# Kernel optimization log

Measured on AMD Instinct MI355X. Metric: run time of the kernel, lower is better.

## Reference

```python
import jax, jax.numpy as jnp
from jax import lax
import numpy as np

FEAT = 256
B = 16
T = 4096
BETA = 1.0


def setup_inputs() -> dict:
    key = jax.random.key(0)
    k0, k1, k2 = jax.random.split(key, 3)
    encoder_outputs = jax.random.normal(k0, (B, T, FEAT), dtype=jnp.float32)
    # Conv1d weight: (out_ch, in_ch, kernel)
    conv_w = jax.random.normal(k1, (FEAT, FEAT, 5), dtype=jnp.float32) * 0.02
    conv_b = jnp.zeros((FEAT,), dtype=jnp.float32)
    lin_w = jax.random.normal(k2, (FEAT, 1), dtype=jnp.float32) * 0.05
    lin_b = jnp.zeros((1,), dtype=jnp.float32)
    return {"encoder_outputs": encoder_outputs, "conv_w": conv_w,
            "conv_b": conv_b, "lin_w": lin_w, "lin_b": lin_b}


def _alphas(x, conv_w, conv_b, lin_w, lin_b):
    # x: [B, T, D] -> alphas [B, T]
    xc = jnp.transpose(x, (0, 2, 1))  # NCH
    y = lax.conv_general_dilated(xc, conv_w, window_strides=(1,),
                                 padding='SAME',
                                 dimension_numbers=('NCH', 'OIH', 'NCH'))
    y = y + conv_b[None, :, None]
    y = jnp.transpose(y, (0, 2, 1))  # [B, T, D]
    return jax.nn.sigmoid(y @ lin_w + lin_b)[..., 0]  # [B, T]


def _cif_single(alpha, h, beta):
    # alpha: [T], h: [T, D]  integrate-and-fire scan
    D = h.shape[-1]
    Tlen = alpha.shape[0]

    def step(carry, inp):
        acc, hacc = carry
        a, hu = inp
        acc_new = acc + a
        fire = acc_new >= beta
        a1 = 1.0 - acc          # mass to complete current segment
        c = hacc + a1 * hu      # emitted segment vector (if fired)
        a2 = a - a1             # leftover mass starting next segment
        acc_out = jnp.where(fire, a2, acc_new)
        hacc_out = jnp.where(fire, a2 * hu, hacc + a * hu)
        return (acc_out, hacc_out), (fire, jnp.where(fire, c, jnp.zeros_like(c)))

    init = (jnp.zeros((), h.dtype), jnp.zeros((D,), h.dtype))
    (acc_f, hacc_f), (fires, cs) = lax.scan(step, init, (alpha, h))

    # pack fired emissions densely; non-fired steps scatter into dump slot Tlen
    idx = jnp.cumsum(fires.astype(jnp.int32)) - 1
    idx = jnp.where(fires, idx, Tlen)
    out = jnp.zeros((Tlen + 1, D), h.dtype).at[idx].add(cs)[:Tlen]
    n = fires.sum().astype(jnp.int32)
    # if no segment fired, emit the final accumulator (torch: c=[h_accum[-1]])
    out = out.at[0].set(jnp.where(n == 0, hacc_f, out[0]))
    n = jnp.maximum(n, 1)
    return out, n


def reference(encoder_outputs, conv_w, conv_b, lin_w, lin_b):
    alphas = _alphas(encoder_outputs, conv_w, conv_b, lin_w, lin_b)  # [B, T]
    out_c, len_tensor = jax.vmap(lambda a, h: _cif_single(a, h, BETA))(
        alphas, encoder_outputs)
    return out_c, len_tensor
```

## Files before the change

kernel.cpp:

```cpp
#include <hip/hip_runtime.h>
#include <math.h>

#define FEAT 256
#define NB   16
#define TLEN 4096
#define NROWS (NB * TLEN)

#define OFF_WEFF 0
#define OFF_BEFF 1280
#define OFF_P    2048
#define OFF_W1   (OFF_P + 5 * NROWS)
#define OFF_W2   (OFF_W1 + NROWS)
#define OFF_FPOS (OFF_W2 + NROWS)
#define OFF_NF   (OFF_FPOS + NROWS)
#define OFF_PART (OFF_NF + 16)
#define OFF_ALPHA (OFF_PART + 8 * 1280)
#define OFF_CSUM (OFF_ALPHA + NROWS)

__global__ __launch_bounds__(256) void weff1_kernel(
    const float* __restrict__ conv_w, const float* __restrict__ lin_w,
    float* __restrict__ ws) {
  int ob = blockIdx.x % 5, oc = blockIdx.x / 5;
  int idx = ob * 256 + threadIdx.x;
  float acc = 0.f;
  int o0 = oc * 32;
#pragma unroll 8
  for (int o = o0; o < o0 + 32; ++o)
    acc = fmaf(conv_w[o * (FEAT * 5) + idx], lin_w[o], acc);
  ws[OFF_PART + oc * 1280 + idx] = acc;
}

__global__ __launch_bounds__(256) void weff2_kernel(
    const float* __restrict__ conv_b, const float* __restrict__ lin_w,
    const float* __restrict__ lin_b, float* __restrict__ ws) {
  if (blockIdx.x < 5) {
    int idx = blockIdx.x * 256 + threadIdx.x;
    float acc = 0.f;
#pragma unroll
    for (int c = 0; c < 8; ++c) acc += ws[OFF_PART + c * 1280 + idx];
    int i = idx / 5, k = idx - i * 5;
    ws[OFF_WEFF + k * FEAT + i] = acc;
  } else {
    __shared__ float red[256];
    red[threadIdx.x] = conv_b[threadIdx.x] * lin_w[threadIdx.x];
    __syncthreads();
    for (int s = 128; s > 0; s >>= 1) {
      if (threadIdx.x < s) red[threadIdx.x] += red[threadIdx.x + s];
      __syncthreads();
    }
    if (threadIdx.x == 0) ws[OFF_BEFF] = red[0] + lin_b[0];
  }
}

__global__ __launch_bounds__(256) void pdot_kernel(
    const float* __restrict__ x, float* __restrict__ ws) {
  int tid  = threadIdx.x;
  int wave = tid >> 6, l = tid & 63;
  int row  = blockIdx.x * 32 + wave * 8 + (l >> 3);
  int l8   = l & 7;
  const float* xr = x + (size_t)row * FEAT + l8 * 4;
  float p[5] = {0.f, 0.f, 0.f, 0.f, 0.f};
#pragma unroll
  for (int pass = 0; pass < 8; ++pass) {
    float4 xv = *(const float4*)(xr + pass * 32);
#pragma unroll
    for (int k = 0; k < 5; ++k) {
      float4 w4 = *(const float4*)(ws + OFF_WEFF + k * FEAT + pass * 32 + l8 * 4);
      p[k] = fmaf(xv.x, w4.x, fmaf(xv.y, w4.y,
              fmaf(xv.z, w4.z, fmaf(xv.w, w4.w, p[k]))));
    }
  }
#pragma unroll
  for (int k = 0; k < 5; ++k) {
    p[k] += __shfl_xor(p[k], 1);
    p[k] += __shfl_xor(p[k], 2);
    p[k] += __shfl_xor(p[k], 4);
  }
  if (l8 == 0) {
#pragma unroll
    for (int k = 0; k < 5; ++k) ws[OFF_P + (size_t)k * NROWS + row] = p[k];
  }
}

__global__ __launch_bounds__(256) void scanA_kernel(float* __restrict__ ws) {
  const int b = blockIdx.x >> 4, chunk = blockIdx.x & 15;
  const int tid = threadIdx.x;
  const int t = chunk * 256 + tid;
  float z = ws[OFF_BEFF];
#pragma unroll
  for (int k = 0; k < 5; ++k) {
    int tt = t + k - 2;
    if (tt >= 0 && tt < TLEN) z += ws[OFF_P + (size_t)k * NROWS + b * TLEN + tt];
  }
  float a = 1.f / (1.f + expf(-z));
  ws[OFF_ALPHA + b * TLEN + t] = a;

  __shared__ double sS[256];
  sS[tid] = (double)a;
  __syncthreads();
  for (int s = 1; s < 256; s <<= 1) {
    double add = (tid >= s) ? sS[tid - s] : 0.0;
    __syncthreads();
    sS[tid] += add;
    __syncthreads();
  }
  if (tid == 255)
    ((double*)ws)[OFF_CSUM / 2 + b * 16 + chunk] = sS[255];
}

__global__ __launch_bounds__(256) void scanB_kernel(
    float* __restrict__ ws, float* __restrict__ out) {
  const int b = blockIdx.x >> 4, chunk = blockIdx.x & 15;
  const int tid = threadIdx.x;
  const int t = chunk * 256 + tid;
  const double* csum = (const double*)ws + OFF_CSUM / 2 + b * 16;
  double offset = 0.0;
  for (int c = 0; c < chunk; ++c) offset += csum[c];

  double a = (double)ws[OFF_ALPHA + b * TLEN + t];
  __shared__ double sS[256];
  sS[tid] = a;
  __syncthreads();
  for (int s = 1; s < 256; s <<= 1) {
    double add = (tid >= s) ? sS[tid - s] : 0.0;
    __syncthreads();
    sS[tid] += add;
    __syncthreads();
  }
  double St = offset + sS[tid];
  double Sp = tid ? offset + sS[tid - 1] : offset;
  double Ft = floor(St), Fp = floor(Sp);

  ws[OFF_W1 + b * TLEN + t] = (float)(fmin(St, Fp + 1.0) - Sp);
  if (Ft > Fp) {
    ws[OFF_W2 + b * TLEN + t] = (float)(St - Ft);
    ((int*)ws)[OFF_FPOS + b * TLEN + (int)Ft - 1] = t;
  }
  if (chunk == 15 && tid == 255) {
    int n = (int)Ft;
    ((int*)ws)[OFF_NF + b] = n;
    out[(size_t)NROWS * FEAT + b] = (float)(n > 0 ? n : 1);
  }
}

__global__ __launch_bounds__(256) void emit_kernel(
    const float* __restrict__ x, const float* __restrict__ ws,
    float* __restrict__ out) {
  int gtid = blockIdx.x * 256 + threadIdx.x;
  int row  = gtid >> 6;
  int lane = gtid & 63;
  int b = row >> 12;
  int j = row & (TLEN - 1);
  int n = ((const int*)ws)[OFF_NF + b];
  int keep = n > 0 ? n : 1;
  float4 acc = make_float4(0.f, 0.f, 0.f, 0.f);
  if (j < keep) {
    const int* fpos = (const int*)ws + OFF_FPOS + b * TLEN;
    int t_lo = j ? fpos[j - 1] : 0;
    int t_hi = (j < n) ? fpos[j] : TLEN - 1;
    const float* w1 = ws + OFF_W1 + b * TLEN;
    const float* w2 = ws + OFF_W2 + b * TLEN;
    for (int t = t_lo; t <= t_hi; ++t) {
      float w = (j && t == t_lo) ? w2[t] : w1[t];
      float4 xv = *(const float4*)(x + ((size_t)b * TLEN + t) * FEAT + lane * 4);
      acc.x = fmaf(w, xv.x, acc.x);
      acc.y = fmaf(w, xv.y, acc.y);
      acc.z = fmaf(w, xv.z, acc.z);
      acc.w = fmaf(w, xv.w, acc.w);
    }
  }
  *(float4*)(out + (size_t)row * FEAT + lane * 4) = acc;
}

extern "C" void kernel_launch(void* const* d_in, const int* in_sizes, int n_in,
                              void* d_out, int out_size, void* d_ws, size_t ws_size,
                              hipStream_t stream) {
  const float* x      = (const float*)d_in[0];
  const float* conv_w = (const float*)d_in[1];
  const float* conv_b = (const float*)d_in[2];
  const float* lin_w  = (const float*)d_in[3];
  const float* lin_b  = (const float*)d_in[4];
  float* out = (float*)d_out;
  float* ws  = (float*)d_ws;

  hipLaunchKernelGGL(weff1_kernel, dim3(40), dim3(256), 0, stream,
                     conv_w, lin_w, ws);
  hipLaunchKernelGGL(weff2_kernel, dim3(6), dim3(256), 0, stream,
                     conv_b, lin_w, lin_b, ws);
  hipLaunchKernelGGL(pdot_kernel, dim3(NROWS / 32), dim3(256), 0, stream, x, ws);
  hipLaunchKernelGGL(scanA_kernel, dim3(NB * 16), dim3(256), 0, stream, ws);
  hipLaunchKernelGGL(scanB_kernel, dim3(NB * 16), dim3(256), 0, stream, ws, out);
  hipLaunchKernelGGL(emit_kernel, dim3(NROWS / 4), dim3(256), 0, stream, x, ws, out);
}
```

Before: 154.8 us.

## Fuse weight reduction, conv-dot and sigmoid; single-block per-batch scan

Merges the bias reduction into the first weight kernel. The partial-sum reduction moves into a new kernel that computes the 5-tap dot products for a 128-row tile with halo, applies the conv window and sigmoid in shared memory, and writes alpha directly, removing the P buffer round trip. The two-pass chunked scan is replaced by one 1024-thread block per batch scanning all 4096 elements in shared memory in double precision. This cuts the launch count from 6 to 4 and removes intermediate global traffic. In exchange, halo rows are reread, each block redundantly re-reduces the weights, and the scan runs on only 16 blocks with 12 log-steps of block-wide barriers.

```diff
diff --git a/kernel.cpp b/kernel.cpp
--- a/kernel.cpp
+++ b/kernel.cpp
@@ -6,40 +6,27 @@
 #define TLEN 4096
 #define NROWS (NB * TLEN)
 
-#define OFF_WEFF 0
-#define OFF_BEFF 1280
-#define OFF_P    2048
-#define OFF_W1   (OFF_P + 5 * NROWS)
-#define OFF_W2   (OFF_W1 + NROWS)
-#define OFF_FPOS (OFF_W2 + NROWS)
-#define OFF_NF   (OFF_FPOS + NROWS)
-#define OFF_PART (OFF_NF + 16)
+#define OFF_BEFF  0
+#define OFF_PART  2
 #define OFF_ALPHA (OFF_PART + 8 * 1280)
-#define OFF_CSUM (OFF_ALPHA + NROWS)
+#define OFF_W1    (OFF_ALPHA + NROWS)
+#define OFF_W2    (OFF_W1 + NROWS)
+#define OFF_FPOS  (OFF_W2 + NROWS)
+#define OFF_NF    (OFF_FPOS + NROWS)
 
 __global__ __launch_bounds__(256) void weff1_kernel(
-    const float* __restrict__ conv_w, const float* __restrict__ lin_w,
+    const float* __restrict__ conv_w, const float* __restrict__ conv_b,
+    const float* __restrict__ lin_w, const float* __restrict__ lin_b,
     float* __restrict__ ws) {
-  int ob = blockIdx.x % 5, oc = blockIdx.x / 5;
-  int idx = ob * 256 + threadIdx.x;
-  float acc = 0.f;
-  int o0 = oc * 32;
+  if (blockIdx.x < 40) {
+    int ob = blockIdx.x % 5, oc = blockIdx.x / 5;
+    int idx = ob * 256 + threadIdx.x;
+    float acc = 0.f;
+    int o0 = oc * 32;
 #pragma unroll 8
-  for (int o = o0; o < o0 + 32; ++o)
-    acc = fmaf(conv_w[o * (FEAT * 5) + idx], lin_w[o], acc);
-  ws[OFF_PART + oc * 1280 + idx] = acc;
-}
-
-__global__ __launch_bounds__(256) void weff2_kernel(
-    const float* __restrict__ conv_b, const float* __restrict__ lin_w,
-    const float* __restrict__ lin_b, float* __restrict__ ws) {
-  if (blockIdx.x < 5) {
-    int idx = blockIdx.x * 256 + threadIdx.x;
-    float acc = 0.f;
-#pragma unroll
-    for (int c = 0; c < 8; ++c) acc += ws[OFF_PART + c * 1280 + idx];
-    int i = idx / 5, k = idx - i * 5;
-    ws[OFF_WEFF + k * FEAT + i] = acc;
+    for (int o = o0; o < o0 + 32; ++o)
+      acc = fmaf(conv_w[o * (FEAT * 5) + idx], lin_w[o], acc);
+    ws[OFF_PART + oc * 1280 + idx] = acc;
   } else {
     __shared__ float red[256];
     red[threadIdx.x] = conv_b[threadIdx.x] * lin_w[threadIdx.x];
@@ -52,94 +39,127 @@
   }
 }
 
-__global__ __launch_bounds__(256) void pdot_kernel(
+__global__ __launch_bounds__(256) void pdalpha_kernel(
     const float* __restrict__ x, float* __restrict__ ws) {
-  int tid  = threadIdx.x;
-  int wave = tid >> 6, l = tid & 63;
-  int row  = blockIdx.x * 32 + wave * 8 + (l >> 3);
-  int l8   = l & 7;
-  const float* xr = x + (size_t)row * FEAT + l8 * 4;
-  float p[5] = {0.f, 0.f, 0.f, 0.f, 0.f};
-#pragma unroll
-  for (int pass = 0; pass < 8; ++pass) {
-    float4 xv = *(const float4*)(xr + pass * 32);
+  __shared__ float sW[5 * 256];
+  __shared__ float sP[5 * 132];
+  const int tid = threadIdx.x;
+
+#pragma unroll
+  for (int j = 0; j < 5; ++j) {
+    int idx = j * 256 + tid;
+    float acc = 0.f;
+#pragma unroll
+    for (int c = 0; c < 8; ++c) acc += ws[OFF_PART + c * 1280 + idx];
+    int i = idx / 5, k = idx - i * 5;
+    sW[k * 256 + i] = acc;
+  }
+  const float b_eff = ws[OFF_BEFF];
+  __syncthreads();
+
+  const int t0 = blockIdx.x * 128;
+  const int bs = (t0 >> 12) << 12;
+  const int be = bs + TLEN;
+  const int lo = t0 - 2;
+  const int start = lo < bs ? bs : lo;
+  const int end0  = t0 + 130;
+  const int end   = end0 > be ? be : end0;
+  const int cnt   = end - start;
+
+  const int wave = tid >> 6, l = tid & 63, l8 = l & 7, g8 = l >> 3;
+  float p[5][5];
+#pragma unroll
+  for (int rp = 0; rp < 5; ++rp)
+#pragma unroll
+    for (int k = 0; k < 5; ++k) p[rp][k] = 0.f;
+
+  int j0 = wave * 8 + g8;
+#pragma unroll
+  for (int fp = 0; fp < 8; ++fp) {
+    float4 w4[5];
+#pragma unroll
+    for (int k = 0; k < 5; ++k)
+      w4[k] = *(const float4*)&sW[k * 256 + fp * 32 + l8 * 4];
+#pragma unroll
+    for (int rp = 0; rp < 5; ++rp) {
+      int j = rp * 32 + j0;
+      if (j < cnt) {
+        float4 xv = *(const float4*)(x + (size_t)(start + j) * FEAT + fp * 32 + l8 * 4);
+#pragma unroll
+        for (int k = 0; k < 5; ++k)
+          p[rp][k] = fmaf(xv.x, w4[k].x, fmaf(xv.y, w4[k].y,
+                      fmaf(xv.z, w4[k].z, fmaf(xv.w, w4[k].w, p[rp][k]))));
+      }
+    }
+  }
+#pragma unroll
+  for (int rp = 0; rp < 5; ++rp) {
+    int j = rp * 32 + j0;
 #pragma unroll
     for (int k = 0; k < 5; ++k) {
-      float4 w4 = *(const float4*)(ws + OFF_WEFF + k * FEAT + pass * 32 + l8 * 4);
-      p[k] = fmaf(xv.x, w4.x, fmaf(xv.y, w4.y,
-              fmaf(xv.z, w4.z, fmaf(xv.w, w4.w, p[k]))));
-    }
-  }
-#pragma unroll
-  for (int k = 0; k < 5; ++k) {
-    p[k] += __shfl_xor(p[k], 1);
-    p[k] += __shfl_xor(p[k], 2);
-    p[k] += __shfl_xor(p[k], 4);
-  }
-  if (l8 == 0) {
-#pragma unroll
-    for (int k = 0; k < 5; ++k) ws[OFF_P + (size_t)k * NROWS + row] = p[k];
-  }
-}
-
-__global__ __launch_bounds__(256) void scanA_kernel(float* __restrict__ ws) {
-  const int b = blockIdx.x >> 4, chunk = blockIdx.x & 15;
+      p[rp][k] += __shfl_xor(p[rp][k], 1);
+      p[rp][k] += __shfl_xor(p[rp][k], 2);
+      p[rp][k] += __shfl_xor(p[rp][k], 4);
+    }
+    if (l8 == 0 && j < cnt) {
+      int jl = (start + j) - lo;
+#pragma unroll
+      for (int k = 0; k < 5; ++k) sP[k * 132 + jl] = p[rp][k];
+    }
+  }
+  __syncthreads();
+
+  if (tid < 128) {
+    int t = t0 + tid;
+    float z = b_eff;
+#pragma unroll
+    for (int k = 0; k < 5; ++k) {
+      int tt = t + k - 2;
+      if (tt >= bs && tt < be) z += sP[k * 132 + (tt - lo)];
+    }
+    ws[OFF_ALPHA + t] = 1.f / (1.f + expf(-z));
+  }
+}
+
+__global__ __launch_bounds__(1024) void scan_kernel(
+    float* __restrict__ ws, float* __restrict__ out) {
+  const int b = blockIdx.x;
   const int tid = threadIdx.x;
-  const int t = chunk * 256 + tid;
-  float z = ws[OFF_BEFF];
-#pragma unroll
-  for (int k = 0; k < 5; ++k) {
-    int tt = t + k - 2;
-    if (tt >= 0 && tt < TLEN) z += ws[OFF_P + (size_t)k * NROWS + b * TLEN + tt];
-  }
-  float a = 1.f / (1.f + expf(-z));
-  ws[OFF_ALPHA + b * TLEN + t] = a;
-
-  __shared__ double sS[256];
-  sS[tid] = (double)a;
+  __shared__ double sS[TLEN];
+#pragma unroll
+  for (int r = 0; r < 4; ++r) {
+    int t = r * 1024 + tid;
+    sS[t] = (double)ws[OFF_ALPHA + b * TLEN + t];
+  }
   __syncthreads();
-  for (int s = 1; s < 256; s <<= 1) {
-    double add = (tid >= s) ? sS[tid - s] : 0.0;
+  for (int s = 1; s < TLEN; s <<= 1) {
+    double add[4];
+#pragma unroll
+    for (int r = 0; r < 4; ++r) {
+      int t = r * 1024 + tid;
+      add[r] = (t >= s) ? sS[t - s] : 0.0;
+    }
     __syncthreads();
-    sS[tid] += add;
+#pragma unroll
+    for (int r = 0; r < 4; ++r) sS[r * 1024 + tid] += add[r];
     __syncthreads();
   }
-  if (tid == 255)
-    ((double*)ws)[OFF_CSUM / 2 + b * 16 + chunk] = sS[255];
-}
-
-__global__ __launch_bounds__(256) void scanB_kernel(
-    float* __restrict__ ws, float* __restrict__ out) {
-  const int b = blockIdx.x >> 4, chunk = blockIdx.x & 15;
-  const int tid = threadIdx.x;
-  const int t = chunk * 256 + tid;
-  const double* csum = (const double*)ws + OFF_CSUM / 2 + b * 16;
-  double offset = 0.0;
-  for (int c = 0; c < chunk; ++c) offset += csum[c];
-
-  double a = (double)ws[OFF_ALPHA + b * TLEN + t];
-  __shared__ double sS[256];
-  sS[tid] = a;
-  __syncthreads();
-  for (int s = 1; s < 256; s <<= 1) {
-    double add = (tid >= s) ? sS[tid - s] : 0.0;
-    __syncthreads();
-    sS[tid] += add;
-    __syncthreads();
-  }
-  double St = offset + sS[tid];
-  double Sp = tid ? offset + sS[tid - 1] : offset;
-  double Ft = floor(St), Fp = floor(Sp);
-
-  ws[OFF_W1 + b * TLEN + t] = (float)(fmin(St, Fp + 1.0) - Sp);
-  if (Ft > Fp) {
-    ws[OFF_W2 + b * TLEN + t] = (float)(St - Ft);
-    ((int*)ws)[OFF_FPOS + b * TLEN + (int)Ft - 1] = t;
-  }
-  if (chunk == 15 && tid == 255) {
-    int n = (int)Ft;
-    ((int*)ws)[OFF_NF + b] = n;
-    out[(size_t)NROWS * FEAT + b] = (float)(n > 0 ? n : 1);
+#pragma unroll
+  for (int r = 0; r < 4; ++r) {
+    int t = r * 1024 + tid;
+    double St = sS[t];
+    double Sp = t ? sS[t - 1] : 0.0;
+    double Ft = floor(St), Fp = floor(Sp);
+    ws[OFF_W1 + b * TLEN + t] = (float)(fmin(St, Fp + 1.0) - Sp);
+    if (Ft > Fp) {
+      ws[OFF_W2 + b * TLEN + t] = (float)(St - Ft);
+      ((int*)ws)[OFF_FPOS + b * TLEN + (int)Ft - 1] = t;
+    }
+    if (t == TLEN - 1) {
+      int n = (int)Ft;
+      ((int*)ws)[OFF_NF + b] = n;
+      out[(size_t)NROWS * FEAT + b] = (float)(n > 0 ? n : 1);
+    }
   }
 }
 
@@ -183,12 +203,9 @@
   float* out = (float*)d_out;
   float* ws  = (float*)d_ws;
 
-  hipLaunchKernelGGL(weff1_kernel, dim3(40), dim3(256), 0, stream,
-                     conv_w, lin_w, ws);
-  hipLaunchKernelGGL(weff2_kernel, dim3(6), dim3(256), 0, stream,
-                     conv_b, lin_w, lin_b, ws);
-  hipLaunchKernelGGL(pdot_kernel, dim3(NROWS / 32), dim3(256), 0, stream, x, ws);
-  hipLaunchKernelGGL(scanA_kernel, dim3(NB * 16), dim3(256), 0, stream, ws);
-  hipLaunchKernelGGL(scanB_kernel, dim3(NB * 16), dim3(256), 0, stream, ws, out);
+  hipLaunchKernelGGL(weff1_kernel, dim3(41), dim3(256), 0, stream,
+                     conv_w, conv_b, lin_w, lin_b, ws);
+  hipLaunchKernelGGL(pdalpha_kernel, dim3(NROWS / 128), dim3(256), 0, stream, x, ws);
+  hipLaunchKernelGGL(scan_kernel, dim3(NB), dim3(1024), 0, stream, ws, out);
   hipLaunchKernelGGL(emit_kernel, dim3(NROWS / 4), dim3(256), 0, stream, x, ws, out);
 }
```

New measurement: 161.2 us. 1.04x slower.
